# Optimization experiments

Hardware: AMD Instinct MI355X
Metric: run time of the kernel (lower is better)

## Reference

```python
import jax, jax.numpy as jnp
import numpy as np
import math

D_MODEL, D_K, D_V, N_HEADS = 1024, 64, 64, 16

def setup_inputs() -> dict:
    key = jax.random.key(0)
    ks = jax.random.split(key, 5)
    x = jax.random.normal(ks[0], (4, 2048, D_MODEL), dtype=jnp.float32)
    s = 1.0 / math.sqrt(D_MODEL)
    # per-head projection weights, stacked: [H, D, d_k] (equivalent to H separate nn.Linear(D, d_k, bias=False))
    Wq = jax.random.normal(ks[1], (N_HEADS, D_MODEL, D_K), dtype=jnp.float32) * s
    Wk = jax.random.normal(ks[2], (N_HEADS, D_MODEL, D_K), dtype=jnp.float32) * s
    Wv = jax.random.normal(ks[3], (N_HEADS, D_MODEL, D_V), dtype=jnp.float32) * s
    # output projection: Linear(d_value*n_heads, d_model, bias=False) -> [H*d_v, D]
    Wo = jax.random.normal(ks[4], (N_HEADS * D_V, D_MODEL), dtype=jnp.float32) * (1.0 / math.sqrt(N_HEADS * D_V))
    return {"x": x, "Wq": Wq, "Wk": Wk, "Wv": Wv, "Wo": Wo}

def reference(x, Wq, Wk, Wv, Wo):
    d_k = Wq.shape[-1]
    # batched per-head projections (fuses the per-head Python loop into one einsum)
    Q = jnp.einsum('bsd,hdk->bhsk', x, Wq)
    K = jnp.einsum('bsd,hdk->bhsk', x, Wk)
    V = jnp.einsum('bsd,hdv->bhsv', x, Wv)
    scores = jnp.einsum('bhqk,bhsk->bhqs', Q, K) / jnp.sqrt(jnp.asarray(d_k, x.dtype))
    weights = jax.nn.softmax(scores, axis=-1)
    heads = jnp.einsum('bhqs,bhsv->bhqv', weights, V)
    B, H, S, Dv = heads.shape
    # concat heads along last dim (head-major order, matching torch.cat of per-head outputs)
    concat = jnp.transpose(heads, (0, 2, 1, 3)).reshape(B, S, H * Dv)
    return concat @ Wo
```

## Files before the change

### kernel.cpp

```cpp
#include <hip/hip_runtime.h>


typedef __attribute__((ext_vector_type(8))) short bf16x8;
typedef __attribute__((ext_vector_type(4))) float f32x4;
typedef __attribute__((ext_vector_type(4))) unsigned short ushortx4;
typedef __attribute__((ext_vector_type(2))) unsigned int uint2v;

__device__ __forceinline__ unsigned short f2bf(float x) {
    unsigned int u = __float_as_uint(x);
    u += 0x7FFFu + ((u >> 16) & 1u);
    return (unsigned short)(u >> 16);
}
__device__ __forceinline__ unsigned int pack_bf2(float hi, float lo) {
    return __builtin_amdgcn_perm(__float_as_uint(hi), __float_as_uint(lo), 0x07060302u);
}

__device__ __forceinline__ void gload_lds16(const unsigned short* g, unsigned short* lds) {
    __builtin_amdgcn_global_load_lds(
        (const __attribute__((address_space(1))) unsigned int*)g,
        (__attribute__((address_space(3))) unsigned int*)lds,
        16, 0, 0);
}

__global__ __launch_bounds__(256) void pack_all(
    const float* __restrict__ x,
    const float* __restrict__ Wq,
    const float* __restrict__ Wk,
    const float* __restrict__ Wv,
    const float* __restrict__ Wo,
    unsigned short* __restrict__ XB,
    unsigned short* __restrict__ WQKVT,
    unsigned short* __restrict__ WOT)
{
    const int bid = blockIdx.x;
    bf16x8 v;
    if (bid < 4096) {
        size_t base = ((size_t)bid * 256 + threadIdx.x) * 8;
        float4 f0 = *(const float4*)&x[base];
        float4 f1 = *(const float4*)&x[base + 4];
        v[0] = f2bf(f0.x); v[1] = f2bf(f0.y); v[2] = f2bf(f0.z); v[3] = f2bf(f0.w);
        v[4] = f2bf(f1.x); v[5] = f2bf(f1.y); v[6] = f2bf(f1.z); v[7] = f2bf(f1.w);
        *(bf16x8*)&XB[base] = v;
    } else if (bid < 5632) {
        int i = (bid - 4096) * 256 + threadIdx.x;
        int d0 = (i * 8) & 1023;
        int n  = (i * 8) >> 10;
        int part = n >> 10;
        int hkk  = n & 1023;
        int h = hkk >> 6, kk = hkk & 63;
        const float* W = (part == 0) ? Wq : ((part == 1) ? Wk : Wv);
        float scale = (part == 0) ? 0.125f * 1.44269504088896f : 1.0f;
        #pragma unroll
        for (int e = 0; e < 8; ++e)
            v[e] = f2bf(W[(h << 16) + ((d0 + e) << 6) + kk] * scale);
        *(bf16x8*)&WQKVT[(size_t)n * 1024 + d0] = v;
    } else {
        int i = (bid - 5632) * 256 + threadIdx.x;
        int k0 = (i * 8) & 1023;
        int n  = (i * 8) >> 10;
        #pragma unroll
        for (int e = 0; e < 8; ++e)
            v[e] = f2bf(Wo[(size_t)(k0 + e) * 1024 + n]);
        *(bf16x8*)&WOT[(size_t)n * 1024 + k0] = v;
    }
}

template<int CMODE, int BN>
__global__ __launch_bounds__(256) void gemm_bt(
    const unsigned short* __restrict__ A,
    const unsigned short* __restrict__ Bt,
    void* __restrict__ Cv,
    unsigned short* __restrict__ VT,
    int M, int N, int K, int ldc)
{
    __shared__ __align__(16) unsigned short As[2][128 * 32];
    __shared__ __align__(16) unsigned short Bs[2][BN * 32];
    const int m0 = blockIdx.y * 128;
    const int n0 = blockIdx.x * BN;
    const int tid  = threadIdx.x;
    const int w    = tid >> 6, lane = tid & 63;
    const int q4   = lane >> 4, lr  = lane & 15;
    constexpr int MI = (BN == 128) ? 4 : 2;
    const int rowBase = (BN == 128) ? (w >> 1) * 64 : w * 32;
    const int colBase = (BN == 128) ? (w & 1) * 64 : 0;

    const int ch   = tid & 3;
    const int row0 = tid >> 2;
    const int ldsOff = w * 512;

    const unsigned short* aP0 = &A [(size_t)(m0 + row0)      * K + ch * 8];
    const unsigned short* aP1 = &A [(size_t)(m0 + row0 + 64) * K + ch * 8];
    const unsigned short* bP0 = &Bt[(size_t)(n0 + row0)      * K + ch * 8];
    const unsigned short* bP1 = (BN == 128)
        ? &Bt[(size_t)(n0 + row0 + 64) * K + ch * 8] : nullptr;

    auto dma = [&](int buf, int k0) {
        gload_lds16(aP0 + k0, &As[buf][ldsOff]);
        gload_lds16(aP1 + k0, &As[buf][2048 + ldsOff]);
        gload_lds16(bP0 + k0, &Bs[buf][ldsOff]);
        if (BN == 128)
            gload_lds16(bP1 + k0, &Bs[buf][2048 + ldsOff]);
    };

    f32x4 acc[MI][4] = {};
    dma(0, 0);
    int cur = 0;

    for (int k0 = 0; k0 < K; k0 += 32) {
        __syncthreads();
        if (k0 + 32 < K) dma(cur ^ 1, k0 + 32);

        bf16x8 af[MI], bfv[4];
        #pragma unroll
        for (int i = 0; i < MI; ++i)
            af[i] = *(const bf16x8*)&As[cur][(rowBase + i * 16 + lr) * 32 + q4 * 8];
        #pragma unroll
        for (int j = 0; j < 4; ++j)
            bfv[j] = *(const bf16x8*)&Bs[cur][(colBase + j * 16 + lr) * 32 + q4 * 8];
        #pragma unroll
        for (int i = 0; i < MI; ++i)
            #pragma unroll
            for (int j = 0; j < 4; ++j)
                acc[i][j] = __builtin_amdgcn_mfma_f32_16x16x32_bf16(af[i], bfv[j], acc[i][j], 0, 0, 0);
        cur ^= 1;
    }

    #pragma unroll
    for (int i = 0; i < MI; ++i) {
        const int row = m0 + rowBase + i * 16 + q4 * 4;
        #pragma unroll
        for (int j = 0; j < 4; ++j) {
            const int col = n0 + colBase + j * 16 + lr;
            if (CMODE == 0) {
                float* C = (float*)Cv;
                #pragma unroll
                for (int p = 0; p < 4; ++p)
                    C[(size_t)(row + p) * ldc + col] = acc[i][j][p];
            } else {
                if (col < 2048) {
                    unsigned short* C = (unsigned short*)Cv;
                    #pragma unroll
                    for (int p = 0; p < 4; ++p)
                        C[(size_t)(row + p) * 2048 + col] = f2bf(acc[i][j][p]);
                } else {
                    const int c2 = col - 2048;
                    const int hh = c2 >> 6, dd = c2 & 63;
                    const int bb = row >> 11, ss = row & 2047;
                    ushortx4 v;
                    #pragma unroll
                    for (int p = 0; p < 4; ++p) v[p] = f2bf(acc[i][j][p]);
                    *(ushortx4*)&VT[((size_t)(bb * 16 + hh) * 64 + dd) * 2048 + ss] = v;
                }
            }
        }
    }
}

__global__ __launch_bounds__(256, 2) void attn_flash(
    const unsigned short* __restrict__ QK,
    const unsigned short* __restrict__ VT,
    unsigned short* __restrict__ HC)
{
    const int bh  = blockIdx.x;
    const int qb  = blockIdx.y;
    const int b   = bh >> 4, h = bh & 15;
    const int tid = threadIdx.x;
    const int w   = tid >> 6, lane = tid & 63;
    const int q4  = lane >> 4, lr  = lane & 15;

    __shared__ __align__(16) unsigned short Ks [2][64 * 64];
    __shared__ __align__(16) unsigned short Vts[2][64 * 64];

    const int drow   = tid >> 3;
    const int gchunk = (tid & 7) ^ (drow & 7);
    const unsigned short* Kg = QK + (size_t)(b * 2048) * 2048 + 1024 + h * 64;
    const unsigned short* Vg = VT + (size_t)bh * 64 * 2048;
    const unsigned short* kP0 = Kg + (size_t)(drow)      * 2048 + gchunk * 8;
    const unsigned short* kP1 = Kg + (size_t)(drow + 32) * 2048 + gchunk * 8;
    const unsigned short* vP0 = Vg + (size_t)(drow)      * 2048 + gchunk * 8;
    const unsigned short* vP1 = Vg + (size_t)(drow + 32) * 2048 + gchunk * 8;
    const int ldsOff = w * 512;

    auto dma = [&](int buf, int t) {
        gload_lds16(kP0 + (size_t)t * 131072, &Ks [buf][ldsOff]);
        gload_lds16(kP1 + (size_t)t * 131072, &Ks [buf][2048 + ldsOff]);
        gload_lds16(vP0 + t * 64,             &Vts[buf][ldsOff]);
        gload_lds16(vP1 + t * 64,             &Vts[buf][2048 + ldsOff]);
    };

    dma(0, 0);

    const int qrow0 = b * 2048 + qb * 256 + w * 64;
    bf16x8 qf[4][2];
    #pragma unroll
    for (int u = 0; u < 4; ++u)
        #pragma unroll
        for (int c = 0; c < 2; ++c)
            qf[u][c] = *(const bf16x8*)&QK[(size_t)(qrow0 + u * 16 + lr) * 2048
                                           + h * 64 + c * 32 + q4 * 8];

    const int lr7 = lr & 7;

    const short oneb = (short)0x3F80;
    const bf16x8 onesf = { oneb, oneb, oneb, oneb, oneb, oneb, oneb, oneb };

    f32x4 o[4][4] = {};
    f32x4 lsum[4] = {};
    int cur = 0;

    for (int t = 0; t < 32; ++t) {
        __syncthreads();
        if (t + 1 < 32) dma(cur ^ 1, t + 1);

        #pragma unroll
        for (int kc = 0; kc < 2; ++kc) {
            unsigned int pk[4][2][2];
            #pragma unroll
            for (int ml = 0; ml < 2; ++ml) {
                const int mt = kc * 2 + ml;
                f32x4 st[4] = {};
                #pragma unroll
                for (int c = 0; c < 2; ++c) {
                    const int slot = (c * 4 + q4) ^ lr7;
                    bf16x8 kf = *(const bf16x8*)&Ks[cur][(mt * 16 + lr) * 64 + slot * 8];
                    #pragma unroll
                    for (int u = 0; u < 4; ++u)
                        st[u] = __builtin_amdgcn_mfma_f32_16x16x32_bf16(kf, qf[u][c], st[u], 0, 0, 0);
                }
                #pragma unroll
                for (int u = 0; u < 4; ++u) {
                    float e0 = __builtin_amdgcn_exp2f(st[u][0]);
                    float e1 = __builtin_amdgcn_exp2f(st[u][1]);
                    float e2 = __builtin_amdgcn_exp2f(st[u][2]);
                    float e3 = __builtin_amdgcn_exp2f(st[u][3]);
                    pk[u][ml][0] = pack_bf2(e1, e0);
                    pk[u][ml][1] = pack_bf2(e3, e2);
                }
            }

            bf16x8 pb[4];
            #pragma unroll
            for (int u = 0; u < 4; ++u) {
                uint2v a0 = __builtin_amdgcn_permlane32_swap(pk[u][0][0], pk[u][1][0], false, false);
                uint2v b0 = __builtin_amdgcn_permlane16_swap(a0[0], a0[1], false, false);
                uint2v a1 = __builtin_amdgcn_permlane32_swap(pk[u][0][1], pk[u][1][1], false, false);
                uint2v b1 = __builtin_amdgcn_permlane16_swap(a1[0], a1[1], false, false);
                int4 wv;
                wv.x = (int)b0[0];
                wv.y = (int)b1[0];
                wv.z = (int)b0[1];
                wv.w = (int)b1[1];
                pb[u] = *(bf16x8*)&wv;
            }

            #pragma unroll
            for (int u = 0; u < 4; ++u)
                lsum[u] = __builtin_amdgcn_mfma_f32_16x16x32_bf16(onesf, pb[u], lsum[u], 0, 0, 0);
            #pragma unroll
            for (int jd = 0; jd < 4; ++jd) {
                const int slot = (kc * 4 + q4) ^ lr7;
                bf16x8 vf = *(const bf16x8*)&Vts[cur][(jd * 16 + lr) * 64 + slot * 8];
                #pragma unroll
                for (int u = 0; u < 4; ++u)
                    o[u][jd] = __builtin_amdgcn_mfma_f32_16x16x32_bf16(vf, pb[u], o[u][jd], 0, 0, 0);
            }
        }
        cur ^= 1;
    }

    #pragma unroll
    for (int u = 0; u < 4; ++u) {
        const float inv = __builtin_amdgcn_rcpf(lsum[u][0]);
        const size_t rowO = (size_t)(qrow0 + u * 16 + lr);
        #pragma unroll
        for (int jd = 0; jd < 4; ++jd) {
            ushortx4 v;
            #pragma unroll
            for (int p = 0; p < 4; ++p)
                v[p] = f2bf(o[u][jd][p] * inv);
            *(ushortx4*)&HC[rowO * 1024 + h * 64 + jd * 16 + q4 * 4] = v;
        }
    }
}

extern "C" void kernel_launch(void* const* d_in, const int* in_sizes, int n_in,
                              void* d_out, int out_size, void* d_ws, size_t ws_size,
                              hipStream_t stream)
{
    const float* x  = (const float*)d_in[0];
    const float* Wq = (const float*)d_in[1];
    const float* Wk = (const float*)d_in[2];
    const float* Wv = (const float*)d_in[3];
    const float* Wo = (const float*)d_in[4];
    float* out = (float*)d_out;

    char* ws = (char*)d_ws;
    unsigned short* XB    = (unsigned short*)(ws);
    unsigned short* HC    = (unsigned short*)(ws);
    unsigned short* WQKVT = (unsigned short*)(ws + 16777216);
    unsigned short* WOT   = (unsigned short*)(ws + 23068672);
    unsigned short* QK    = (unsigned short*)(ws + 25165824);
    unsigned short* VT    = (unsigned short*)(ws + 58720256);

    pack_all<<<6144, 256, 0, stream>>>(x, Wq, Wk, Wv, Wo, XB, WQKVT, WOT);
    gemm_bt<1, 128><<<dim3(24, 64), 256, 0, stream>>>(XB, WQKVT, QK, VT, 8192, 3072, 1024, 0);
    attn_flash<<<dim3(64, 8), 256, 0, stream>>>(QK, VT, HC);
    gemm_bt<0, 64><<<dim3(16, 64), 256, 0, stream>>>(HC, WOT, out, nullptr, 8192, 1024, 1024, 1024);
}
```

Before: 285.7 us.

## Transpose weights via LDS tiles and halve attention query rows per block

The weight packing now stages 64x128 tiles in LDS so that global reads and writes are both coalesced, replacing the strided per-element gathers. The block count drops to match. The attention kernel also handles 32 query rows per wave instead of 64, doubles the grid and raises launch bounds to 4 blocks per CU, aiming for more occupancy and a better fill of the 256 CUs. The cost is that each K/V tile loaded into LDS is reused by half as many query rows, so more total K/V traffic.

New measurement: 266.5 us. 6.7% less time.

```diff
diff --git a/kernel.cpp b/kernel.cpp
--- a/kernel.cpp
+++ b/kernel.cpp
@@ -33,35 +33,68 @@
     unsigned short* __restrict__ WOT)
 {
     const int bid = blockIdx.x;
-    bf16x8 v;
+    const int tid = threadIdx.x;
     if (bid < 4096) {
-        size_t base = ((size_t)bid * 256 + threadIdx.x) * 8;
+        bf16x8 v;
+        size_t base = ((size_t)bid * 256 + tid) * 8;
         float4 f0 = *(const float4*)&x[base];
         float4 f1 = *(const float4*)&x[base + 4];
         v[0] = f2bf(f0.x); v[1] = f2bf(f0.y); v[2] = f2bf(f0.z); v[3] = f2bf(f0.w);
         v[4] = f2bf(f1.x); v[5] = f2bf(f1.y); v[6] = f2bf(f1.z); v[7] = f2bf(f1.w);
         *(bf16x8*)&XB[base] = v;
-    } else if (bid < 5632) {
-        int i = (bid - 4096) * 256 + threadIdx.x;
-        int d0 = (i * 8) & 1023;
-        int n  = (i * 8) >> 10;
-        int part = n >> 10;
-        int hkk  = n & 1023;
-        int h = hkk >> 6, kk = hkk & 63;
+        return;
+    }
+
+    __shared__ float lds[64 * 129];
+    const float* src;
+    size_t outbase;
+    float scale = 1.0f;
+    int instride;
+    unsigned short* outp;
+    if (bid < 4480) {
+        const int widx = bid - 4096;
+        const int part = widx >> 7;
+        const int rem  = widx & 127;
+        const int h    = rem >> 3;
+        const int chunk = rem & 7;
         const float* W = (part == 0) ? Wq : ((part == 1) ? Wk : Wv);
-        float scale = (part == 0) ? 0.125f * 1.44269504088896f : 1.0f;
+        src = W + h * 65536 + chunk * 8192;
+        instride = 64;
+        outbase = ((size_t)(part * 1024 + h * 64)) * 1024 + chunk * 128;
+        if (part == 0) scale = 0.125f * 1.44269504088896f;
+        outp = WQKVT;
+    } else {
+        const int oidx = bid - 4480;
+        const int kc = oidx >> 4;
+        const int nc = oidx & 15;
+        src = Wo + (size_t)kc * 128 * 1024 + nc * 64;
+        instride = 1024;
+        outbase = (size_t)(nc * 64) * 1024 + kc * 128;
+        outp = WOT;
+    }
+
+    const int r0 = tid >> 4;
+    const int c4 = (tid & 15) * 4;
+    #pragma unroll
+    for (int cc = 0; cc < 8; ++cc) {
+        const int r = cc * 16 + r0;
+        float4 f = *(const float4*)&src[(size_t)r * instride + c4];
+        lds[(c4 + 0) * 129 + r] = f.x * scale;
+        lds[(c4 + 1) * 129 + r] = f.y * scale;
+        lds[(c4 + 2) * 129 + r] = f.z * scale;
+        lds[(c4 + 3) * 129 + r] = f.w * scale;
+    }
+    __syncthreads();
+
+    const int c = tid >> 2;
+    const int s = tid & 3;
+    #pragma unroll
+    for (int j = 0; j < 4; ++j) {
+        bf16x8 v;
         #pragma unroll
         for (int e = 0; e < 8; ++e)
-            v[e] = f2bf(W[(h << 16) + ((d0 + e) << 6) + kk] * scale);
-        *(bf16x8*)&WQKVT[(size_t)n * 1024 + d0] = v;
-    } else {
-        int i = (bid - 5632) * 256 + threadIdx.x;
-        int k0 = (i * 8) & 1023;
-        int n  = (i * 8) >> 10;
-        #pragma unroll
-        for (int e = 0; e < 8; ++e)
-            v[e] = f2bf(Wo[(size_t)(k0 + e) * 1024 + n]);
-        *(bf16x8*)&WOT[(size_t)n * 1024 + k0] = v;
+            v[e] = f2bf(lds[c * 129 + s * 32 + j * 8 + e]);
+        *(bf16x8*)&outp[outbase + (size_t)c * 1024 + s * 32 + j * 8] = v;
     }
 }
 
@@ -156,7 +189,7 @@
     }
 }
 
-__global__ __launch_bounds__(256, 2) void attn_flash(
+__global__ __launch_bounds__(256, 4) void attn_flash(
     const unsigned short* __restrict__ QK,
     const unsigned short* __restrict__ VT,
     unsigned short* __restrict__ HC)
@@ -190,10 +223,10 @@
 
     dma(0, 0);
 
-    const int qrow0 = b * 2048 + qb * 256 + w * 64;
-    bf16x8 qf[4][2];
-    #pragma unroll
-    for (int u = 0; u < 4; ++u)
+    const int qrow0 = b * 2048 + qb * 128 + w * 32;
+    bf16x8 qf[2][2];
+    #pragma unroll
+    for (int u = 0; u < 2; ++u)
         #pragma unroll
         for (int c = 0; c < 2; ++c)
             qf[u][c] = *(const bf16x8*)&QK[(size_t)(qrow0 + u * 16 + lr) * 2048
@@ -204,8 +237,8 @@
     const short oneb = (short)0x3F80;
     const bf16x8 onesf = { oneb, oneb, oneb, oneb, oneb, oneb, oneb, oneb };
 
-    f32x4 o[4][4] = {};
-    f32x4 lsum[4] = {};
+    f32x4 o[2][4] = {};
+    f32x4 lsum[2] = {};
     int cur = 0;
 
     for (int t = 0; t < 32; ++t) {
@@ -214,21 +247,21 @@
 
         #pragma unroll
         for (int kc = 0; kc < 2; ++kc) {
-            unsigned int pk[4][2][2];
+            unsigned int pk[2][2][2];
             #pragma unroll
             for (int ml = 0; ml < 2; ++ml) {
                 const int mt = kc * 2 + ml;
-                f32x4 st[4] = {};
+                f32x4 st[2] = {};
                 #pragma unroll
                 for (int c = 0; c < 2; ++c) {
                     const int slot = (c * 4 + q4) ^ lr7;
                     bf16x8 kf = *(const bf16x8*)&Ks[cur][(mt * 16 + lr) * 64 + slot * 8];
                     #pragma unroll
-                    for (int u = 0; u < 4; ++u)
+                    for (int u = 0; u < 2; ++u)
                         st[u] = __builtin_amdgcn_mfma_f32_16x16x32_bf16(kf, qf[u][c], st[u], 0, 0, 0);
                 }
                 #pragma unroll
-                for (int u = 0; u < 4; ++u) {
+                for (int u = 0; u < 2; ++u) {
                     float e0 = __builtin_amdgcn_exp2f(st[u][0]);
                     float e1 = __builtin_amdgcn_exp2f(st[u][1]);
                     float e2 = __builtin_amdgcn_exp2f(st[u][2]);
@@ -238,9 +271,9 @@
                 }
             }
 
-            bf16x8 pb[4];
-            #pragma unroll
-            for (int u = 0; u < 4; ++u) {
+            bf16x8 pb[2];
+            #pragma unroll
+            for (int u = 0; u < 2; ++u) {
                 uint2v a0 = __builtin_amdgcn_permlane32_swap(pk[u][0][0], pk[u][1][0], false, false);
                 uint2v b0 = __builtin_amdgcn_permlane16_swap(a0[0], a0[1], false, false);
                 uint2v a1 = __builtin_amdgcn_permlane32_swap(pk[u][0][1], pk[u][1][1], false, false);
@@ -254,14 +287,14 @@
             }
 
             #pragma unroll
-            for (int u = 0; u < 4; ++u)
+            for (int u = 0; u < 2; ++u)
                 lsum[u] = __builtin_amdgcn_mfma_f32_16x16x32_bf16(onesf, pb[u], lsum[u], 0, 0, 0);
             #pragma unroll
             for (int jd = 0; jd < 4; ++jd) {
                 const int slot = (kc * 4 + q4) ^ lr7;
                 bf16x8 vf = *(const bf16x8*)&Vts[cur][(jd * 16 + lr) * 64 + slot * 8];
                 #pragma unroll
-                for (int u = 0; u < 4; ++u)
+                for (int u = 0; u < 2; ++u)
                     o[u][jd] = __builtin_amdgcn_mfma_f32_16x16x32_bf16(vf, pb[u], o[u][jd], 0, 0, 0);
             }
         }
@@ -269,7 +302,7 @@
     }
 
     #pragma unroll
-    for (int u = 0; u < 4; ++u) {
+    for (int u = 0; u < 2; ++u) {
         const float inv = __builtin_amdgcn_rcpf(lsum[u][0]);
         const size_t rowO = (size_t)(qrow0 + u * 16 + lr);
         #pragma unroll
@@ -302,8 +335,8 @@
     unsigned short* QK    = (unsigned short*)(ws + 25165824);
     unsigned short* VT    = (unsigned short*)(ws + 58720256);
 
-    pack_all<<<6144, 256, 0, stream>>>(x, Wq, Wk, Wv, Wo, XB, WQKVT, WOT);
+    pack_all<<<4608, 256, 0, stream>>>(x, Wq, Wk, Wv, Wo, XB, WQKVT, WOT);
     gemm_bt<1, 128><<<dim3(24, 64), 256, 0, stream>>>(XB, WQKVT, QK, VT, 8192, 3072, 1024, 0);
-    attn_flash<<<dim3(64, 8), 256, 0, stream>>>(QK, VT, HC);
+    attn_flash<<<dim3(64, 16), 256, 0, stream>>>(QK, VT, HC);
     gemm_bt<0, 64><<<dim3(16, 64), 256, 0, stream>>>(HC, WOT, out, nullptr, 8192, 1024, 1024, 1024);
 }
```
